# Optimization experiments

Measured on AMD Instinct MI355X. Metric: run time of the kernel, lower is better.

## Reference

```python
import jax, jax.numpy as jnp
import numpy as np

N = 256        # ImageSize
NC = 8         # coils
NSPOKE = 34    # radial spokes
NVEC = 512     # samples per spoke
K = NSPOKE * NVEC  # total k-space points


def setup_inputs() -> dict:
    key = jax.random.key(0)
    k1, k2, k3, k4 = jax.random.split(key, 4)
    input_r = jax.random.normal(k1, (N, N, 2), dtype=jnp.float32)
    C_r = jax.random.normal(k2, (NC, N, N, 2), dtype=jnp.float32)
    w = jax.random.uniform(k3, (NVEC,), dtype=jnp.float32)
    # nonuniform k-space coordinates in [-pi, pi)
    angle = jax.random.uniform(k4, (K, 2), dtype=jnp.float32,
                               minval=-np.pi, maxval=np.pi)
    return {"input_r": input_r, "C_r": C_r, "w": w, "angle": angle}


def reference(input_r, C_r, w, angle):
    # Type-3 NUFFT: y[c,k] = sum_j C[c,j]*x[j] * exp(-i*(s_k*(-x1_j) + t_k*(-x2_j)))
    #             = sum_{a,b} (C[c,a,b]*x[a,b]) * exp(+i*s_k*g[a]) * exp(+i*t_k*g[b])
    # since the source grid is separable: x1_j = g[a], x2_j = g[b],
    # g = linspace(-N//2, N//2-1, N) for even N (iflag=0 -> negative sign).
    n = input_r.shape[0]
    nvec = w.shape[0]
    g = jnp.arange(n, dtype=jnp.float32) - n // 2          # [N]

    x = input_r[..., 0] + 1j * input_r[..., 1]             # [N,N] complex64
    C = C_r[..., 0] + 1j * C_r[..., 1]                     # [Nc,N,N] complex64
    Xc = C * x[None]                                       # coil-weighted image [Nc,N,N]

    s = angle[:, 0]                                        # [K]
    t = angle[:, 1]                                        # [K]
    E1 = jnp.exp(1j * s[:, None] * g[None, :])             # [K,N] phase along axis a
    E2 = jnp.exp(1j * t[:, None] * g[None, :])             # [K,N] phase along axis b

    # contract b first -> [Nc,K,N], then a -> [Nc,K]
    y = jnp.einsum('kb,cab,ka->ck', E2, Xc, E1, optimize=True)  # [Nc,K]

    # density compensation: wr = tile(w, (Nc, Nspoke, 1)).reshape(Nc, -1)
    wr = jnp.tile(w, y.shape[1] // nvec)                   # [K]
    y = y * wr[None, :]

    return jnp.stack([jnp.real(y), jnp.imag(y)], axis=-1)  # [Nc,K,2] float32
```

## Files before the change

### kernel.cpp

```cpp
#include <hip/hip_runtime.h>
#include <hip/hip_bf16.h>
#include <stdint.h>


#define NKTOT 17408
#define NBLK 272
#define NT 8

typedef short bf16x8 __attribute__((ext_vector_type(8)));
typedef float f32x4 __attribute__((ext_vector_type(4)));

__device__ __forceinline__ unsigned short f2bf(float f) {
  unsigned int u = __builtin_bit_cast(unsigned int, f);
  u += 0x7FFFu + ((u >> 16) & 1u);
  return (unsigned short)(u >> 16);
}
__device__ __forceinline__ unsigned int pk2bf(float lo, float hi) {
  return (unsigned int)f2bf(lo) | ((unsigned int)f2bf(hi) << 16);
}

__device__ __forceinline__ void async_copy16(void* lds, const void* g) {
  __builtin_amdgcn_global_load_lds(
      (const __attribute__((address_space(1))) unsigned int*)g,
      (__attribute__((address_space(3))) unsigned int*)lds, 16, 0, 0);
}

__device__ __forceinline__ size_t aidx(int c, int m, int jj) {
  int tt = jj >> 5;
  int s = ((m & 1) << 2) | ((jj >> 3) & 3);
  return (((size_t)(c * 8 + tt) * 256 + (m >> 1)) * 8 + s) * 8 + (jj & 7);
}

__global__ __launch_bounds__(256) void pack_a(
    const float* __restrict__ input_r, const float* __restrict__ C_r,
    unsigned short* __restrict__ Apack, float* __restrict__ biastab)
{
  const int bx = blockIdx.x;
  const int tid = threadIdx.x;
  const int p = bx * 2 + (tid >> 7);
  const int a = p & 255;
  const int c = p >> 8;
  const int j = tid & 127;
  const size_t xbase = (size_t)a * 256;
  const size_t cbase = ((size_t)(c * 256 + a)) * 256;
  if (j == 0) {
    float xr = input_r[(xbase + 128) * 2], xi = input_r[(xbase + 128) * 2 + 1];
    float cr = C_r[(cbase + 128) * 2],     ci = C_r[(cbase + 128) * 2 + 1];
    biastab[c * 512 + a]       = cr * xr - ci * xi;
    biastab[c * 512 + 256 + a] = cr * xi + ci * xr;
    xr = input_r[xbase * 2]; xi = input_r[xbase * 2 + 1];
    cr = C_r[cbase * 2];     ci = C_r[cbase * 2 + 1];
    float reb = cr * xr - ci * xi, imb = cr * xi + ci * xr;
    Apack[aidx(c, a, 127)]       = f2bf(reb);
    Apack[aidx(c, a, 255)]       = f2bf(imb);
    Apack[aidx(c, 256 + a, 127)] = f2bf(imb);
    Apack[aidx(c, 256 + a, 255)] = f2bf(-reb);
  } else {
    const int bp = 128 + j, bm = 128 - j;
    float xpr = input_r[(xbase + bp) * 2], xpi = input_r[(xbase + bp) * 2 + 1];
    float cpr = C_r[(cbase + bp) * 2],     cpi = C_r[(cbase + bp) * 2 + 1];
    float pr = cpr * xpr - cpi * xpi, pi = cpr * xpi + cpi * xpr;
    float xmr = input_r[(xbase + bm) * 2], xmi = input_r[(xbase + bm) * 2 + 1];
    float cmr = C_r[(cbase + bm) * 2],     cmi = C_r[(cbase + bm) * 2 + 1];
    float mrv = cmr * xmr - cmi * xmi, miv = cmr * xmi + cmi * xmr;
    Apack[aidx(c, a, j - 1)]         = f2bf(pr + mrv);
    Apack[aidx(c, a, 127 + j)]       = f2bf(miv - pi);
    Apack[aidx(c, 256 + a, j - 1)]   = f2bf(pi + miv);
    Apack[aidx(c, 256 + a, 127 + j)] = f2bf(pr - mrv);
  }
}

__device__ __forceinline__ void b_compute(unsigned short* buf, float2 et,
                                          float t, int tile, int w, int l,
                                          int bwoff) {
  const float jb = (float)((tile & 3) * 32 + w * 4 + 1);
  float s0, c0;
  __sincosf(t * jb, &s0, &c0);
  float c1 = c0 * et.x - s0 * et.y, s1 = s0 * et.x + c0 * et.y;
  float c2 = c1 * et.x - s1 * et.y, s2 = s1 * et.x + c1 * et.y;
  float c3 = c2 * et.x - s2 * et.y, s3 = s2 * et.x + c2 * et.y;
  const bool use_cos = tile < 4;
  float v0 = use_cos ? c0 : s0;
  float v1 = use_cos ? c1 : s1;
  float v2 = use_cos ? c2 : s2;
  float v3 = use_cos ? c3 : s3;
  uint2 pk;
  pk.x = pk2bf(v0, v1);
  pk.y = pk2bf(v2, v3);
  *(uint2*)(buf + bwoff) = pk;
}

__global__ __launch_bounds__(512, 4) void gemm_fused(
    const unsigned short* __restrict__ Apack,
    const float* __restrict__ biastab,
    const float* __restrict__ angle,
    const float* __restrict__ wvec,
    float* __restrict__ out)
{
  __shared__ unsigned short As[2][16384];
  __shared__ unsigned short Bs[2][2048];
  __shared__ float scol[8][2][64];
  float2* const etbuf = (float2*)&scol[0][0][0];

  const int bx = blockIdx.x;
  const int c = (bx >> 3) & 7;
  const int ktile = (bx >> 6) * 8 + (bx & 7);
  const int kt0 = ktile * 64;
  const int tid = threadIdx.x;
  const int w = tid >> 6;
  const int l = tid & 63;
  const int lhi = l >> 4;
  const int llo = l & 15;
  const int lr = l >> 3;
  const int lsw = ((l & 7) ^ lr) * 8;

  const unsigned short* Aimg = Apack + (size_t)c * (8 * 16384);
  const float* biasp = biastab + c * 512 + w * 64 + lhi * 4;

  const int u8 = ((((llo & 1) << 2) | lhi) ^ ((llo >> 1) & 7)) * 8;
  const int plbase = llo >> 1;

  const float t_reg = angle[(size_t)(kt0 + l) * 2 + 1];
  const int bwoff = (l >> 1) * 64 +
      ((((l & 1) << 2) | (w >> 1)) ^ ((l >> 1) & 7)) * 8 + (w & 1) * 4;

  f32x4 acc[4][4];
#pragma unroll
  for (int fi = 0; fi < 4; ++fi) {
    f32x4 b4 = *(const f32x4*)(biasp + fi * 16);
#pragma unroll
    for (int fj = 0; fj < 4; ++fj) acc[fi][fj] = b4;
  }

#pragma unroll
  for (int i = 0; i < 4; ++i) {
    int row0 = (w * 4 + i) * 8;
    async_copy16(&As[0][row0 * 64], Aimg + (size_t)(row0 + lr) * 64 + lsw);
  }
  {
    float2 et0;
    __sincosf(t_reg, &et0.y, &et0.x);
    etbuf[tid] = et0;
    b_compute(&Bs[0][0], et0, t_reg, 0, w, l, bwoff);
  }
  __syncthreads();

#pragma unroll 2
  for (int tt = 0; tt < NT; ++tt) {
    const int cu = tt & 1;
    if (tt < NT - 1) {
      const unsigned short* Asrc = Aimg + (size_t)(tt + 1) * 16384;
#pragma unroll
      for (int i = 0; i < 4; ++i) {
        int row0 = (w * 4 + i) * 8;
        async_copy16(&As[cu ^ 1][row0 * 64],
                     Asrc + (size_t)(row0 + lr) * 64 + lsw);
      }
    }
    __builtin_amdgcn_sched_barrier(0);

    bf16x8 bfr[4];
#pragma unroll
    for (int fj = 0; fj < 4; ++fj)
      bfr[fj] = *(const bf16x8*)&Bs[cu][(fj * 8 + plbase) * 64 + u8];
    bf16x8 af[4];
#pragma unroll
    for (int fi = 0; fi < 4; ++fi)
      af[fi] = *(const bf16x8*)&As[cu][(w * 32 + fi * 8 + plbase) * 64 + u8];
#pragma unroll
    for (int fi = 0; fi < 4; ++fi)
#pragma unroll
      for (int fj = 0; fj < 4; ++fj)
        acc[fi][fj] = __builtin_amdgcn_mfma_f32_16x16x32_bf16(
            af[fi], bfr[fj], acc[fi][fj], 0, 0, 0);

    if (tt < NT - 1) {
      float2 et = etbuf[tid];
      b_compute(&Bs[cu ^ 1][0], et, t_reg, tt + 1, w, l, bwoff);
    }
    __syncthreads();
  }

  const int aoff = (w & 3) * 64;
  const float a0f = (float)(aoff + lhi * 4 - 128);
#pragma unroll
  for (int fj = 0; fj < 4; ++fj) {
    const int col = fj * 16 + llo;
    const int k = kt0 + col;
    const float s = angle[(size_t)k * 2];
    float s1, c1, sY, cY;
    __sincosf(s, &s1, &c1);
    __sincosf(16.f * s, &sY, &cY);
    float c2 = c1 * c1 - s1 * s1, s2 = 2.f * c1 * s1;
    float c3 = c2 * c1 - s2 * s1, s3 = c2 * s1 + s2 * c1;
    float cY2 = cY * cY - sY * sY, sY2 = 2.f * cY * sY;
    float cY3 = cY2 * cY - sY2 * sY, sY3 = cY2 * sY + sY2 * cY;
    const float Yr[4] = {1.f, cY, cY2, cY3};
    const float Yi[4] = {0.f, sY, sY2, sY3};
    float Or = 0.f, Oi = 0.f;
#pragma unroll
    for (int fi = 0; fi < 4; ++fi) {
      float v0 = acc[fi][fj][0], v1 = acc[fi][fj][1];
      float v2 = acc[fi][fj][2], v3 = acc[fi][fj][3];
      float Ir = v0 + c1 * v1 + c2 * v2 + c3 * v3;
      float Ii = s1 * v1 + s2 * v2 + s3 * v3;
      Or += Yr[fi] * Ir - Yi[fi] * Ii;
      Oi += Yi[fi] * Ir + Yr[fi] * Ii;
    }
    float sb, cb;
    __sincosf(s * a0f, &sb, &cb);
    float sumr = cb * Or - sb * Oi;
    float sumi = sb * Or + cb * Oi;
    sumr += __shfl_xor(sumr, 16, 64);
    sumr += __shfl_xor(sumr, 32, 64);
    sumi += __shfl_xor(sumi, 16, 64);
    sumi += __shfl_xor(sumi, 32, 64);
    if (lhi == 0) {
      scol[w][0][col] = sumr;
      scol[w][1][col] = sumi;
    }
  }
  __syncthreads();
  if (tid < 128) {
    const int col = tid >> 1;
    const int comp = tid & 1;
    const int k = kt0 + col;
    float re = scol[0][0][col] + scol[1][0][col] + scol[2][0][col] + scol[3][0][col]
             - scol[4][1][col] - scol[5][1][col] - scol[6][1][col] - scol[7][1][col];
    float im = scol[0][1][col] + scol[1][1][col] + scol[2][1][col] + scol[3][1][col]
             + scol[4][0][col] + scol[5][0][col] + scol[6][0][col] + scol[7][0][col];
    float val = comp ? im : re;
    out[((size_t)c * NKTOT + k) * 2 + comp] = val * wvec[k & 511];
  }
}

extern "C" void kernel_launch(void* const* d_in, const int* in_sizes, int n_in,
                              void* d_out, int out_size, void* d_ws, size_t ws_size,
                              hipStream_t stream) {
  const float* input_r = (const float*)d_in[0];
  const float* C_r     = (const float*)d_in[1];
  const float* wvec    = (const float*)d_in[2];
  const float* angle   = (const float*)d_in[3];
  float* out = (float*)d_out;

  unsigned short* Apack = (unsigned short*)d_ws;
  float* biastab = (float*)((char*)d_ws + (size_t)2097152);

  pack_a<<<1024, 256, 0, stream>>>(input_r, C_r, Apack, biastab);
  gemm_fused<<<8 * NBLK, 512, 0, stream>>>(Apack, biastab, angle, wvec, out);
}
```

Baseline: 116.7 us.

## Load A fragments directly from global into registers, drop LDS staging

Removes the double-buffered LDS staging of the packed A operand and its async global-to-LDS copies. Each lane now reads its bf16x8 A fragments straight from global memory, since every A row is used by only one wave. LDS use per block drops sharply, which may raise occupancy, and the per-lane phase step is kept in a register instead of being round-tripped through LDS. In exchange, global load latency is no longer overlapped by the explicit prefetch and lands directly before the MFMAs, so it relies on occupancy and the cache to hide it.

```diff
diff --git a/kernel.cpp b/kernel.cpp
--- a/kernel.cpp
+++ b/kernel.cpp
@@ -17,12 +17,6 @@
 }
 __device__ __forceinline__ unsigned int pk2bf(float lo, float hi) {
   return (unsigned int)f2bf(lo) | ((unsigned int)f2bf(hi) << 16);
-}
-
-__device__ __forceinline__ void async_copy16(void* lds, const void* g) {
-  __builtin_amdgcn_global_load_lds(
-      (const __attribute__((address_space(1))) unsigned int*)g,
-      (__attribute__((address_space(3))) unsigned int*)lds, 16, 0, 0);
 }
 
 __device__ __forceinline__ size_t aidx(int c, int m, int jj) {
@@ -97,10 +91,8 @@
     const float* __restrict__ wvec,
     float* __restrict__ out)
 {
-  __shared__ unsigned short As[2][16384];
   __shared__ unsigned short Bs[2][2048];
   __shared__ float scol[8][2][64];
-  float2* const etbuf = (float2*)&scol[0][0][0];
 
   const int bx = blockIdx.x;
   const int c = (bx >> 3) & 7;
@@ -111,16 +103,17 @@
   const int l = tid & 63;
   const int lhi = l >> 4;
   const int llo = l & 15;
-  const int lr = l >> 3;
-  const int lsw = ((l & 7) ^ lr) * 8;
-
-  const unsigned short* Aimg = Apack + (size_t)c * (8 * 16384);
+
+  const unsigned short* Alane = Apack + (size_t)c * (8 * 16384)
+      + (size_t)(w * 32 + (llo >> 1)) * 64 + (((llo & 1) << 2) | lhi) * 8;
   const float* biasp = biastab + c * 512 + w * 64 + lhi * 4;
 
   const int u8 = ((((llo & 1) << 2) | lhi) ^ ((llo >> 1) & 7)) * 8;
   const int plbase = llo >> 1;
 
   const float t_reg = angle[(size_t)(kt0 + l) * 2 + 1];
+  float2 et;
+  __sincosf(t_reg, &et.y, &et.x);
   const int bwoff = (l >> 1) * 64 +
       ((((l & 1) << 2) | (w >> 1)) ^ ((l >> 1) & 7)) * 8 + (w & 1) * 4;
 
@@ -132,41 +125,21 @@
     for (int fj = 0; fj < 4; ++fj) acc[fi][fj] = b4;
   }
 
-#pragma unroll
-  for (int i = 0; i < 4; ++i) {
-    int row0 = (w * 4 + i) * 8;
-    async_copy16(&As[0][row0 * 64], Aimg + (size_t)(row0 + lr) * 64 + lsw);
-  }
-  {
-    float2 et0;
-    __sincosf(t_reg, &et0.y, &et0.x);
-    etbuf[tid] = et0;
-    b_compute(&Bs[0][0], et0, t_reg, 0, w, l, bwoff);
-  }
+  b_compute(&Bs[0][0], et, t_reg, 0, w, l, bwoff);
   __syncthreads();
 
 #pragma unroll 2
   for (int tt = 0; tt < NT; ++tt) {
     const int cu = tt & 1;
-    if (tt < NT - 1) {
-      const unsigned short* Asrc = Aimg + (size_t)(tt + 1) * 16384;
-#pragma unroll
-      for (int i = 0; i < 4; ++i) {
-        int row0 = (w * 4 + i) * 8;
-        async_copy16(&As[cu ^ 1][row0 * 64],
-                     Asrc + (size_t)(row0 + lr) * 64 + lsw);
-      }
-    }
-    __builtin_amdgcn_sched_barrier(0);
+    bf16x8 af[4];
+#pragma unroll
+    for (int fi = 0; fi < 4; ++fi)
+      af[fi] = *(const bf16x8*)(Alane + (size_t)tt * 16384 + fi * 512);
 
     bf16x8 bfr[4];
 #pragma unroll
     for (int fj = 0; fj < 4; ++fj)
       bfr[fj] = *(const bf16x8*)&Bs[cu][(fj * 8 + plbase) * 64 + u8];
-    bf16x8 af[4];
-#pragma unroll
-    for (int fi = 0; fi < 4; ++fi)
-      af[fi] = *(const bf16x8*)&As[cu][(w * 32 + fi * 8 + plbase) * 64 + u8];
 #pragma unroll
     for (int fi = 0; fi < 4; ++fi)
 #pragma unroll
@@ -174,10 +147,8 @@
         acc[fi][fj] = __builtin_amdgcn_mfma_f32_16x16x32_bf16(
             af[fi], bfr[fj], acc[fi][fj], 0, 0, 0);
 
-    if (tt < NT - 1) {
-      float2 et = etbuf[tid];
+    if (tt < NT - 1)
       b_compute(&Bs[cu ^ 1][0], et, t_reg, tt + 1, w, l, bwoff);
-    }
     __syncthreads();
   }
 
```

Result: slower. 119.6 us (+2.5%).
